# Optimization experiments

Hardware: AMD Instinct MI355X
Metric: run time of the kernel (lower is better)

The kernel has to match this reference:

```python
import jax, jax.numpy as jnp
import numpy as np

B, DIM, DQ, H, W, K = 64, 64, 8, 64, 64, 64


def setup_inputs() -> dict:
    key = jax.random.key(0)
    k1, k2, k3 = jax.random.split(key, 3)
    features = jax.random.normal(k1, (B, DIM, H, W), dtype=jnp.float32)
    query = jax.random.normal(k2, (B, DQ, H, W), dtype=jnp.float32)
    # Ensemble of K 1x1 convs (Conv2d(dim, dim_query, 1, bias=False)) -> [K, DQ, DIM]
    weight = jax.random.normal(k3, (K, DQ, DIM), dtype=jnp.float32) * (1.0 / np.sqrt(DIM))
    return {"features": features, "query": query, "weight": weight}


def reference(features, query, weight):
    # Ensemble of K 1x1 convs: key_values [k, b, dq, h, w]
    key_values = jnp.einsum('bchw,kqc->kbqhw', features, weight)
    b = query.shape[0]
    q_flat = query.reshape(b, -1)                       # [b, D], D = dq*h*w
    kv_flat = key_values.reshape(K, b, -1)              # [k, b, D]
    # torch.cdist(query[b,1,D], kv[b,k,D]) -> euclidean distance [b, k]
    diff = kv_flat - q_flat[None, :, :]                 # [k, b, D]
    distance = jnp.sqrt(jnp.sum(diff * diff, axis=-1)).T  # [b, k]
    codes = jnp.argmax(-distance, axis=-1)              # [b]
    # gather per-batch selected key_values
    sel_key_values = key_values[codes, jnp.arange(b)]   # [b, dq, h, w]
    commit_loss = jnp.mean((sel_key_values - query) ** 2)
    return sel_key_values, codes, commit_loss
```

## Files before the change

kernel.cpp:

```cpp
#include <hip/hip_runtime.h>

#define BQ   64
#define CDIM 64
#define DQN  8
#define HWN  4096
#define KKN  64

typedef float  f32x4  __attribute__((ext_vector_type(4)));
typedef short  short8 __attribute__((ext_vector_type(8)));

__device__ __forceinline__ ushort f2bf(float x) {
  uint u = __float_as_uint(x);
  u += 0x7fffu + ((u >> 16) & 1u);
  return (ushort)(u >> 16);
}
__device__ __forceinline__ float bf2f(ushort h) {
  return __uint_as_float(((uint)h) << 16);
}

__device__ __forceinline__ void cvtStore(ushort* __restrict__ H,
                                         ushort* __restrict__ L,
                                         int uoff, float4 f) {
  ushort4 h = make_ushort4((ushort)(__float_as_uint(f.x) >> 16),
                           (ushort)(__float_as_uint(f.y) >> 16),
                           (ushort)(__float_as_uint(f.z) >> 16),
                           (ushort)(__float_as_uint(f.w) >> 16));
  ushort4 l = make_ushort4(f2bf(f.x - bf2f(h.x)), f2bf(f.y - bf2f(h.y)),
                           f2bf(f.z - bf2f(h.z)), f2bf(f.w - bf2f(h.w)));
  *(ushort4*)(H + uoff) = h;
  *(ushort4*)(L + uoff) = l;
}

__global__ __launch_bounds__(256, 4) void k_gram(const float* __restrict__ feat,
                                                 const float* __restrict__ qry,
                                                 float* __restrict__ part, int chb) {
  __shared__ ushort ldsH[80 * 128];
  __shared__ ushort ldsL[80 * 128];
  int tid = threadIdx.x;
  int wv = tid >> 6, lane = tid & 63;
  int blk = blockIdx.x;
  int b = blk / chb, cb = blk - b * chb;
  int CH = 4096 / chb;
  int hwBase = cb * CH;
  int nch = CH >> 7;
  const float* fb = feat + (size_t)b * (CDIM * HWN);
  const float* qb = qry + (size_t)b * (DQN * HWN);

  for (int i = tid; i < 8 * 128; i += 256) {
    ldsH[72 * 128 + i] = 0;
    ldsL[72 * 128 + i] = 0;
  }

  int g4 = tid & 31;
  int r8 = tid >> 5;
  int frow = lane & 15;
  int fk = (lane >> 4) * 8;
  f32x4 acc[5] = {};

  for (int ch = 0; ch < nch; ++ch) {
    int hw0 = hwBase + ch * 128;
    #pragma unroll
    for (int it = 0; it < 9; ++it) {
      int r = it * 8 + r8;
      const float* src = (r < 64) ? (fb + (size_t)r * HWN + hw0 + g4 * 4)
                                  : (qb + (size_t)(r - 64) * HWN + hw0 + g4 * 4);
      float4 f = *(const float4*)src;
      int uoff = r * 128 + ((g4 * 4) ^ ((r & 7) << 3));
      cvtStore(ldsH, ldsL, uoff, f);
    }
    __syncthreads();
    #pragma unroll
    for (int ks = 0; ks < 4; ++ks) {
      short8 fh[5], fl[5];
      #pragma unroll
      for (int t = 0; t < 5; ++t) {
        int row = t * 16 + frow;
        int uo = row * 128 + ((ks * 32 + fk) ^ ((row & 7) << 3));
        fh[t] = *(const short8*)(ldsH + uo);
        fl[t] = *(const short8*)(ldsL + uo);
      }
      short8 bh, bl;
      switch (wv) {
        case 0:  bh = fh[0]; bl = fl[0]; break;
        case 1:  bh = fh[1]; bl = fl[1]; break;
        case 2:  bh = fh[2]; bl = fl[2]; break;
        default: bh = fh[3]; bl = fl[3]; break;
      }
      #pragma unroll
      for (int t = 0; t < 5; ++t) {
        acc[t] = __builtin_amdgcn_mfma_f32_16x16x32_bf16(fh[t], bh, acc[t], 0, 0, 0);
        acc[t] = __builtin_amdgcn_mfma_f32_16x16x32_bf16(fh[t], bl, acc[t], 0, 0, 0);
        acc[t] = __builtin_amdgcn_mfma_f32_16x16x32_bf16(fl[t], bh, acc[t], 0, 0, 0);
      }
    }
    __syncthreads();
  }

  float* op = part + (size_t)blk * 4608 + wv * 16 + (lane & 15);
  int r0 = (lane >> 4) * 4;
  #pragma unroll
  for (int t = 0; t < 5; ++t) {
    #pragma unroll
    for (int r = 0; r < 4; ++r) {
      int row = t * 16 + r0 + r;
      if (row < 72) op[row * 64] = acc[t][r];
    }
  }
}

__global__ __launch_bounds__(256) void k_reduce(const float* __restrict__ part,
                                                float* __restrict__ Sarr,
                                                float* __restrict__ Garr, int chb) {
  int g = blockIdx.x * 256 + threadIdx.x;
  int b = g / 1152;
  int o = (g - b * 1152) * 4;
  f32x4 s = {};
  #pragma unroll 8
  for (int cb = 0; cb < chb; ++cb) {
    f32x4 p = *(const f32x4*)(part + (size_t)(b * chb + cb) * 4608 + o);
    s += p;
  }
  int r = o >> 6, c = o & 63;
  if (r < 64)
    *(f32x4*)(Sarr + b * 4096 + r * 64 + c) = s;
  else
    *(f32x4*)(Garr + b * 512 + (r - 64) * 64 + c) = s;
}

__global__ __launch_bounds__(256) void k_dist(const float* __restrict__ Sarr,
                                              const float* __restrict__ Garr,
                                              const float* __restrict__ wt,
                                              float* __restrict__ dist) {
  __shared__ float wl[4][512];
  int tid = threadIdx.x, wv = tid >> 6, lane = tid & 63;
  int wid = blockIdx.x * 4 + wv;
  int b = wid >> 6, k = wid & 63;
  for (int t = lane; t < 512; t += 64) wl[wv][t] = wt[k * 512 + t];
  __syncthreads();
  const float* Sb = Sarr + b * 4096;
  float v[8] = {};
  #pragma unroll 4
  for (int j = 0; j < 64; ++j) {
    float s = Sb[j * 64 + lane];
    #pragma unroll
    for (int q = 0; q < 8; ++q) v[q] = fmaf(s, wl[wv][q * 64 + j], v[q]);
  }
  double red = 0.0;
  #pragma unroll
  for (int q = 0; q < 8; ++q) {
    float wqi = wl[wv][q * 64 + lane];
    float gqi = Garr[b * 512 + q * 64 + lane];
    red += (double)wqi * ((double)v[q] - 2.0 * (double)gqi);
  }
  #pragma unroll
  for (int off = 32; off; off >>= 1) red += __shfl_xor(red, off);
  if (lane == 0) dist[b * 64 + k] = (float)red;
}

__global__ __launch_bounds__(256) void k_select(const float* __restrict__ feat,
                                                const float* __restrict__ qry,
                                                const float* __restrict__ wt,
                                                const float* __restrict__ dist,
                                                float* __restrict__ outSel,
                                                float* __restrict__ outCodes,
                                                float* __restrict__ lossPart) {
  __shared__ float wl[512];
  __shared__ float lred[4];
  int bid = blockIdx.x, tid = threadIdx.x;
  int b = bid >> 2, chunk = bid & 2 ? (bid & 3) : (bid & 3);
  chunk = bid & 3;
  int lane = tid & 63;
  float d = dist[b * 64 + lane];
  int bi = lane;
  #pragma unroll
  for (int off = 32; off; off >>= 1) {
    float d2 = __shfl_xor(d, off);
    int i2 = __shfl_xor(bi, off);
    if (d2 < d || (d2 == d && i2 < bi)) { d = d2; bi = i2; }
  }
  int code = bi;
  if (chunk == 0 && tid == 0) outCodes[b] = (float)code;
  wl[tid] = wt[code * 512 + tid];
  wl[tid + 256] = wt[code * 512 + 256 + tid];
  __syncthreads();
  int hw = chunk * 1024 + tid * 4;
  const float* fb = feat + (size_t)b * (CDIM * HWN);
  float4 acc[8] = {};
  #pragma unroll 4
  for (int c = 0; c < 64; ++c) {
    float4 f = *(const float4*)(fb + c * HWN + hw);
    #pragma unroll
    for (int q = 0; q < 8; ++q) {
      float w = wl[q * 64 + c];
      acc[q].x = fmaf(w, f.x, acc[q].x);
      acc[q].y = fmaf(w, f.y, acc[q].y);
      acc[q].z = fmaf(w, f.z, acc[q].z);
      acc[q].w = fmaf(w, f.w, acc[q].w);
    }
  }
  float lsum = 0.f;
  #pragma unroll
  for (int q = 0; q < 8; ++q) {
    size_t off = (size_t)b * 32768 + q * 4096 + hw;
    float4 qv = *(const float4*)(qry + off);
    *(float4*)(outSel + off) = acc[q];
    float dx = acc[q].x - qv.x, dy = acc[q].y - qv.y;
    float dz = acc[q].z - qv.z, dw = acc[q].w - qv.w;
    lsum += dx * dx + dy * dy + dz * dz + dw * dw;
  }
  #pragma unroll
  for (int off = 32; off; off >>= 1) lsum += __shfl_xor(lsum, off);
  if ((tid & 63) == 0) lred[tid >> 6] = lsum;
  __syncthreads();
  if (tid == 0) lossPart[bid] = lred[0] + lred[1] + lred[2] + lred[3];
}

__global__ void k_loss(const float* __restrict__ lossPart, float* __restrict__ outLoss) {
  __shared__ float lred[4];
  int tid = threadIdx.x;
  float s = lossPart[tid];
  #pragma unroll
  for (int off = 32; off; off >>= 1) s += __shfl_xor(s, off);
  if ((tid & 63) == 0) lred[tid >> 6] = s;
  __syncthreads();
  if (tid == 0) outLoss[0] = (lred[0] + lred[1] + lred[2] + lred[3]) * (1.0f / 2097152.0f);
}

extern "C" void kernel_launch(void* const* d_in, const int* in_sizes, int n_in,
                              void* d_out, int out_size, void* d_ws, size_t ws_size,
                              hipStream_t stream) {
  const float* feat = (const float*)d_in[0];
  const float* qry  = (const float*)d_in[1];
  const float* wt   = (const float*)d_in[2];
  float* out = (float*)d_out;
  float* sel      = out;
  float* outCodes = out + 2097152;
  float* outLoss  = out + 2097216;

  int chb = 16;
  while (chb > 1 &&
         ((size_t)64 * chb * 4608 + 64 * 4096 + 64 * 512 + 4096 + 256) * 4 > ws_size)
    chb >>= 1;
  float* wsf = (float*)d_ws;
  float* part = wsf;
  float* Sarr = part + (size_t)64 * chb * 4608;
  float* Garr = Sarr + 64 * 4096;
  float* dist = Garr + 64 * 512;
  float* lossPart = dist + 4096;

  k_gram<<<64 * chb, 256, 0, stream>>>(feat, qry, part, chb);
  k_reduce<<<(64 * 1152) / 256, 256, 0, stream>>>(part, Sarr, Garr, chb);
  k_dist<<<1024, 256, 0, stream>>>(Sarr, Garr, wt, dist);
  k_select<<<256, 256, 0, stream>>>(feat, qry, wt, dist, sel, outCodes, lossPart);
  k_loss<<<1, 256, 0, stream>>>(lossPart, outLoss);
}
```

Before: 50.44 us.

## Replace partial-sum buffer and reduce kernel with atomic accumulation; split select finer

The gram kernel now accumulates its per-chunk results directly into the S and G arrays with float atomicAdd, after a small zeroing kernel, instead of writing partials that a separate reduce kernel sums. This removes the partial buffer traffic and one launch, at the cost of 16-way atomic contention per element and a nondeterministic summation order. The select kernel is also split into twice as many blocks, each handling two elements per thread instead of four, to raise parallelism. The loss reduction now reads 512 partials to match.

```diff
diff --git a/kernel.cpp b/kernel.cpp
--- a/kernel.cpp
+++ b/kernel.cpp
@@ -7,6 +7,7 @@
 #define KKN  64
 
 typedef float  f32x4  __attribute__((ext_vector_type(4)));
+typedef float  f32x2  __attribute__((ext_vector_type(2)));
 typedef short  short8 __attribute__((ext_vector_type(8)));
 
 __device__ __forceinline__ ushort f2bf(float x) {
@@ -31,9 +32,15 @@
   *(ushort4*)(L + uoff) = l;
 }
 
+__global__ __launch_bounds__(256) void k_zero(float* __restrict__ p) {
+  int i = blockIdx.x * 256 + threadIdx.x;
+  ((f32x4*)p)[i] = (f32x4){};
+}
+
 __global__ __launch_bounds__(256, 4) void k_gram(const float* __restrict__ feat,
                                                  const float* __restrict__ qry,
-                                                 float* __restrict__ part, int chb) {
+                                                 float* __restrict__ Sarr,
+                                                 float* __restrict__ Garr, int chb) {
   __shared__ ushort ldsH[80 * 128];
   __shared__ ushort ldsL[80 * 128];
   int tid = threadIdx.x;
@@ -96,35 +103,21 @@
     __syncthreads();
   }
 
-  float* op = part + (size_t)blk * 4608 + wv * 16 + (lane & 15);
+  int col = wv * 16 + (lane & 15);
   int r0 = (lane >> 4) * 4;
-  #pragma unroll
-  for (int t = 0; t < 5; ++t) {
-    #pragma unroll
-    for (int r = 0; r < 4; ++r) {
-      int row = t * 16 + r0 + r;
-      if (row < 72) op[row * 64] = acc[t][r];
-    }
-  }
-}
-
-__global__ __launch_bounds__(256) void k_reduce(const float* __restrict__ part,
-                                                float* __restrict__ Sarr,
-                                                float* __restrict__ Garr, int chb) {
-  int g = blockIdx.x * 256 + threadIdx.x;
-  int b = g / 1152;
-  int o = (g - b * 1152) * 4;
-  f32x4 s = {};
-  #pragma unroll 8
-  for (int cb = 0; cb < chb; ++cb) {
-    f32x4 p = *(const f32x4*)(part + (size_t)(b * chb + cb) * 4608 + o);
-    s += p;
-  }
-  int r = o >> 6, c = o & 63;
-  if (r < 64)
-    *(f32x4*)(Sarr + b * 4096 + r * 64 + c) = s;
-  else
-    *(f32x4*)(Garr + b * 512 + (r - 64) * 64 + c) = s;
+  float* Sb = Sarr + b * 4096;
+  float* Gb = Garr + b * 512;
+  #pragma unroll
+  for (int t = 0; t < 4; ++t) {
+    #pragma unroll
+    for (int r = 0; r < 4; ++r)
+      atomicAdd(Sb + (t * 16 + r0 + r) * 64 + col, acc[t][r]);
+  }
+  if (r0 < 8) {
+    #pragma unroll
+    for (int r = 0; r < 4; ++r)
+      atomicAdd(Gb + (r0 + r) * 64 + col, acc[4][r]);
+  }
 }
 
 __global__ __launch_bounds__(256) void k_dist(const float* __restrict__ Sarr,
@@ -167,8 +160,7 @@
   __shared__ float wl[512];
   __shared__ float lred[4];
   int bid = blockIdx.x, tid = threadIdx.x;
-  int b = bid >> 2, chunk = bid & 2 ? (bid & 3) : (bid & 3);
-  chunk = bid & 3;
+  int b = bid >> 3, chunk = bid & 7;
   int lane = tid & 63;
   float d = dist[b * 64 + lane];
   int bi = lane;
@@ -183,30 +175,27 @@
   wl[tid] = wt[code * 512 + tid];
   wl[tid + 256] = wt[code * 512 + 256 + tid];
   __syncthreads();
-  int hw = chunk * 1024 + tid * 4;
+  int hw = chunk * 512 + tid * 2;
   const float* fb = feat + (size_t)b * (CDIM * HWN);
-  float4 acc[8] = {};
+  f32x2 acc[8] = {};
   #pragma unroll 4
   for (int c = 0; c < 64; ++c) {
-    float4 f = *(const float4*)(fb + c * HWN + hw);
+    f32x2 f = *(const f32x2*)(fb + c * HWN + hw);
     #pragma unroll
     for (int q = 0; q < 8; ++q) {
       float w = wl[q * 64 + c];
       acc[q].x = fmaf(w, f.x, acc[q].x);
       acc[q].y = fmaf(w, f.y, acc[q].y);
-      acc[q].z = fmaf(w, f.z, acc[q].z);
-      acc[q].w = fmaf(w, f.w, acc[q].w);
     }
   }
   float lsum = 0.f;
   #pragma unroll
   for (int q = 0; q < 8; ++q) {
     size_t off = (size_t)b * 32768 + q * 4096 + hw;
-    float4 qv = *(const float4*)(qry + off);
-    *(float4*)(outSel + off) = acc[q];
+    f32x2 qv = *(const f32x2*)(qry + off);
+    *(f32x2*)(outSel + off) = acc[q];
     float dx = acc[q].x - qv.x, dy = acc[q].y - qv.y;
-    float dz = acc[q].z - qv.z, dw = acc[q].w - qv.w;
-    lsum += dx * dx + dy * dy + dz * dz + dw * dw;
+    lsum += dx * dx + dy * dy;
   }
   #pragma unroll
   for (int off = 32; off; off >>= 1) lsum += __shfl_xor(lsum, off);
@@ -218,7 +207,7 @@
 __global__ void k_loss(const float* __restrict__ lossPart, float* __restrict__ outLoss) {
   __shared__ float lred[4];
   int tid = threadIdx.x;
-  float s = lossPart[tid];
+  float s = lossPart[tid] + lossPart[tid + 256];
   #pragma unroll
   for (int off = 32; off; off >>= 1) s += __shfl_xor(s, off);
   if ((tid & 63) == 0) lred[tid >> 6] = s;
@@ -238,19 +227,15 @@
   float* outLoss  = out + 2097216;
 
   int chb = 16;
-  while (chb > 1 &&
-         ((size_t)64 * chb * 4608 + 64 * 4096 + 64 * 512 + 4096 + 256) * 4 > ws_size)
-    chb >>= 1;
   float* wsf = (float*)d_ws;
-  float* part = wsf;
-  float* Sarr = part + (size_t)64 * chb * 4608;
+  float* Sarr = wsf;
   float* Garr = Sarr + 64 * 4096;
   float* dist = Garr + 64 * 512;
   float* lossPart = dist + 4096;
 
-  k_gram<<<64 * chb, 256, 0, stream>>>(feat, qry, part, chb);
-  k_reduce<<<(64 * 1152) / 256, 256, 0, stream>>>(part, Sarr, Garr, chb);
+  k_zero<<<288, 256, 0, stream>>>(Sarr);
+  k_gram<<<64 * chb, 256, 0, stream>>>(feat, qry, Sarr, Garr, chb);
   k_dist<<<1024, 256, 0, stream>>>(Sarr, Garr, wt, dist);
-  k_select<<<256, 256, 0, stream>>>(feat, qry, wt, dist, sel, outCodes, lossPart);
+  k_select<<<512, 256, 0, stream>>>(feat, qry, wt, dist, sel, outCodes, lossPart);
   k_loss<<<1, 256, 0, stream>>>(lossPart, outLoss);
 }
```

After: 59.16 us. 1.17x slower.
